# Optimization experiments

Measured on AMD Instinct MI355X. Metric: run time of the kernel, lower is better.

The kernel has to match this reference:

```python
import jax, jax.numpy as jnp
import numpy as np

B, L, H, NH = 8, 1024, 1024, 16
HD = H // NH  # head_dim = 64
SCALE = HD ** -0.5


def setup_inputs() -> dict:
    key = jax.random.key(0)
    kx, kqkv, kw, kb = jax.random.split(key, 4)
    x = jax.random.normal(kx, (B, L, H), dtype=jnp.float32)
    # nn.Linear(H, 3H, bias=False): weight [3H, H]
    w_qkv = jax.random.normal(kqkv, (3 * H, H), dtype=jnp.float32) * (H ** -0.5)
    # out_proj: nn.Linear(H, H) with bias
    w_out = jax.random.normal(kw, (H, H), dtype=jnp.float32) * (H ** -0.5)
    b_out = jax.random.normal(kb, (H,), dtype=jnp.float32) * 0.01
    return {"x": x, "w_qkv": w_qkv, "w_out": w_out, "b_out": b_out}


def reference(x, w_qkv, w_out, b_out):
    # qkv projection: [B, L, 3H]
    qkv = jnp.einsum('bld,ed->ble', x, w_qkv)
    # rearrange 'b l (qkv h d) -> qkv b h l d'
    qkv = qkv.reshape(B, L, 3, NH, HD)
    q = qkv[:, :, 0].transpose(0, 2, 1, 3)  # [B, NH, L, HD]
    k = qkv[:, :, 1].transpose(0, 2, 1, 3)
    v = qkv[:, :, 2].transpose(0, 2, 1, 3)
    att = jnp.einsum('bhxd,bhyd->bhxy', q, k) * SCALE
    att = jax.nn.softmax(att, axis=-1)
    o = jnp.einsum('bhxy,bhyd->bhxd', att, v)  # [B, NH, L, HD]
    o = o.transpose(0, 2, 1, 3).reshape(B, L, H)
    return jnp.einsum('bld,ed->ble', o, w_out) + b_out
```

## Files before the change

### kernel.cpp

```cpp
#include <hip/hip_runtime.h>


typedef short s16x8 __attribute__((ext_vector_type(8)));
typedef float f32x4 __attribute__((ext_vector_type(4)));
typedef unsigned int u32x2 __attribute__((ext_vector_type(2)));
typedef unsigned int u32x4 __attribute__((ext_vector_type(4)));

__device__ __forceinline__ unsigned short f2bf(float f) {
    union { float f; unsigned u; } c; c.f = f;
    return (unsigned short)((c.u + 0x7FFFu + ((c.u >> 16) & 1u)) >> 16);
}
__device__ __forceinline__ unsigned pack2bf(float a, float b) {
    union { float f; unsigned u; } ca, cb; ca.f = a; cb.f = b;
    return __builtin_amdgcn_perm(cb.u + 0x8000u, ca.u + 0x8000u, 0x07060302u);
}

#define GLOAD_LDS(g, l) __builtin_amdgcn_global_load_lds( \
    (const __attribute__((address_space(1))) void*)(g),   \
    (__attribute__((address_space(3))) void*)(l), 16, 0, 0)

__global__ __launch_bounds__(256) void cvt3(
    const float* __restrict__ s0, unsigned short* __restrict__ d0, int n0,
    const float* __restrict__ s1, unsigned short* __restrict__ d1, int n1,
    const float* __restrict__ s2, unsigned short* __restrict__ d2, int n2)
{
    long i = ((long)blockIdx.x * 256 + threadIdx.x) * 8;
    const float* s; unsigned short* d; long off;
    if (i < n0)                  { s = s0; d = d0; off = i; }
    else if (i < (long)n0 + n1)  { s = s1; d = d1; off = i - n0; }
    else                         { s = s2; d = d2; off = i - n0 - n1; }
    f32x4 a = *(const f32x4*)(s + off);
    f32x4 b = *(const f32x4*)(s + off + 4);
    u32x4 r;
    r[0] = pack2bf(a[0], a[1]); r[1] = pack2bf(a[2], a[3]);
    r[2] = pack2bf(b[0], b[1]); r[3] = pack2bf(b[2], b[3]);
    *(u32x4*)(d + off) = r;
}

template<int EPI>
__global__ __launch_bounds__(256) void gemm16(
    const unsigned short* __restrict__ A, const unsigned short* __restrict__ Bm,
    unsigned short* __restrict__ Cq, unsigned short* __restrict__ Cv,
    float* __restrict__ Cf, const float* __restrict__ bias,
    int N, int K)
{
    __shared__ unsigned short As[128 * 32];
    __shared__ unsigned short Bs[128 * 32];
    const int tid = threadIdx.x, lane = tid & 63, wave = tid >> 6;
    const int quad = lane >> 4, l16 = lane & 15;
    const int wm = (wave >> 1) * 64, wn = (wave & 1) * 64;
    const int m0 = blockIdx.y * 128, n0 = blockIdx.x * 128;

    const int lin0 = wave * 128 + lane, lin1 = lin0 + 64;
    const int r0 = lin0 >> 2, r1 = lin1 >> 2;
    const int q0c = (lin0 & 3) ^ ((r0 >> 1) & 3);
    const int q1c = (lin1 & 3) ^ ((r1 >> 1) & 3);
    const unsigned short* gA0 = A + (size_t)(m0 + r0) * K + q0c * 8;
    const unsigned short* gA1 = A + (size_t)(m0 + r1) * K + q1c * 8;
    const unsigned short* gB0 = Bm + (size_t)(n0 + r0) * K + q0c * 8;
    const unsigned short* gB1 = Bm + (size_t)(n0 + r1) * K + q1c * 8;

    const int pc = ((quad ^ ((l16 >> 1) & 3))) * 8;

    f32x4 acc[4][4] = {};
    for (int k0 = 0; k0 < K; k0 += 32) {
        __syncthreads();
        GLOAD_LDS(gA0, As + lin0 * 8);
        GLOAD_LDS(gA1, As + lin1 * 8);
        GLOAD_LDS(gB0, Bs + lin0 * 8);
        GLOAD_LDS(gB1, Bs + lin1 * 8);
        gA0 += 32; gA1 += 32; gB0 += 32; gB1 += 32;
        __syncthreads();
        s16x8 af[4], bf[4];
        #pragma unroll
        for (int i = 0; i < 4; ++i)
            af[i] = *(const s16x8*)(As + (wm + i * 16 + l16) * 32 + pc);
        #pragma unroll
        for (int j = 0; j < 4; ++j)
            bf[j] = *(const s16x8*)(Bs + (wn + j * 16 + l16) * 32 + pc);
        #pragma unroll
        for (int i = 0; i < 4; ++i)
            #pragma unroll
            for (int j = 0; j < 4; ++j)
                acc[i][j] = __builtin_amdgcn_mfma_f32_16x16x32_bf16(af[i], bf[j], acc[i][j], 0, 0, 0);
    }

    if (EPI == 1) {
        #pragma unroll
        for (int j = 0; j < 4; ++j) {
            int col = n0 + wn + j * 16 + l16;
            float bv = bias[col];
            #pragma unroll
            for (int i = 0; i < 4; ++i)
                #pragma unroll
                for (int r = 0; r < 4; ++r)
                    Cf[(size_t)(m0 + wm + i * 16 + quad * 4 + r) * N + col] = acc[i][j][r] + bv;
        }
    } else if (n0 < 2048) {
        #pragma unroll
        for (int j = 0; j < 4; ++j) {
            int col = n0 + wn + j * 16 + l16;
            #pragma unroll
            for (int i = 0; i < 4; ++i)
                #pragma unroll
                for (int r = 0; r < 4; ++r)
                    Cq[(size_t)(m0 + wm + i * 16 + quad * 4 + r) * 2048 + col] = f2bf(acc[i][j][r]);
        }
    } else {
        #pragma unroll
        for (int j = 0; j < 4; ++j) {
            int dcol = n0 + wn + j * 16 + l16 - 2048;
            int hh = dcol >> 6, dd = dcol & 63;
            #pragma unroll
            for (int i = 0; i < 4; ++i)
                #pragma unroll
                for (int r = 0; r < 4; ++r) {
                    int row = m0 + wm + i * 16 + quad * 4 + r;
                    int bb = row >> 10, l = row & 1023;
                    Cv[(size_t)((bb * 16 + hh) * 64 + dd) * 1024 + l] = f2bf(acc[i][j][r]);
                }
        }
    }
}

__global__ __launch_bounds__(256) void attn(
    const unsigned short* __restrict__ qk, const unsigned short* __restrict__ Vt,
    unsigned short* __restrict__ O)
{
    __shared__ unsigned short Ks[64 * 64];
    __shared__ unsigned short Vs[64 * 64];
    __shared__ unsigned short Ps[4][16 * 72];

    const int bh = blockIdx.y, b = bh >> 4, h = bh & 15;
    const int q0 = blockIdx.x * 64;
    const int tid = threadIdx.x, lane = tid & 63, wave = tid >> 6;
    const int quad = lane >> 4, l16 = lane & 15;

    const unsigned short* qrow = qk + (size_t)(b * 1024 + q0 + wave * 16 + l16) * 2048 + h * 64;
    s16x8 qf[2];
    qf[0] = *(const s16x8*)(qrow + quad * 8);
    qf[1] = *(const s16x8*)(qrow + 32 + quad * 8);

    const int rl = lane >> 3;
    const int qc = (lane & 7) ^ rl;
    const int g0 = wave * 2, g1 = g0 + 1;
    const unsigned short* srcK0 = qk + (size_t)(b * 1024 + g0 * 8 + rl) * 2048 + 1024 + h * 64 + qc * 8;
    const unsigned short* srcK1 = qk + (size_t)(b * 1024 + g1 * 8 + rl) * 2048 + 1024 + h * 64 + qc * 8;
    const unsigned short* srcV0 = Vt + (size_t)(bh * 64 + g0 * 8 + rl) * 1024 + qc * 8;
    const unsigned short* srcV1 = Vt + (size_t)(bh * 64 + g1 * 8 + rl) * 1024 + qc * 8;
    unsigned short* dK0 = Ks + g0 * 512 + lane * 8;
    unsigned short* dK1 = Ks + g1 * 512 + lane * 8;
    unsigned short* dV0 = Vs + g0 * 512 + lane * 8;
    unsigned short* dV1 = Vs + g1 * 512 + lane * 8;

    const int sw = l16 & 7;

    f32x4 Oacc[4] = {};
    float lsum = 0.0f;

    for (int kv = 0; kv < 1024; kv += 64) {
        __syncthreads();
        GLOAD_LDS(srcK0, dK0);
        GLOAD_LDS(srcK1, dK1);
        GLOAD_LDS(srcV0, dV0);
        GLOAD_LDS(srcV1, dV1);
        srcK0 += (size_t)64 * 2048; srcK1 += (size_t)64 * 2048;
        srcV0 += 64; srcV1 += 64;
        __syncthreads();

        f32x4 Sacc[4] = {};
        #pragma unroll
        for (int j = 0; j < 4; ++j) {
            #pragma unroll
            for (int s = 0; s < 2; ++s) {
                s16x8 kf = *(const s16x8*)(Ks + (j * 16 + l16) * 64 + (((s * 4 + quad) ^ sw)) * 8);
                Sacc[j] = __builtin_amdgcn_mfma_f32_16x16x32_bf16(kf, qf[s], Sacc[j], 0, 0, 0);
            }
        }

        #pragma unroll
        for (int j = 0; j < 4; ++j) {
            float p0 = __expf(Sacc[j][0] * 0.125f);
            float p1 = __expf(Sacc[j][1] * 0.125f);
            float p2 = __expf(Sacc[j][2] * 0.125f);
            float p3 = __expf(Sacc[j][3] * 0.125f);
            lsum += (p0 + p1) + (p2 + p3);
            u32x2 pw;
            pw[0] = pack2bf(p0, p1);
            pw[1] = pack2bf(p2, p3);
            *(u32x2*)(Ps[wave] + l16 * 72 + j * 16 + quad * 4) = pw;
        }
        asm volatile("s_waitcnt lgkmcnt(0)" ::: "memory");

        #pragma unroll
        for (int s = 0; s < 2; ++s) {
            s16x8 pf = *(const s16x8*)(Ps[wave] + l16 * 72 + s * 32 + quad * 8);
            #pragma unroll
            for (int j = 0; j < 4; ++j) {
                s16x8 vf = *(const s16x8*)(Vs + (j * 16 + l16) * 64 + (((s * 4 + quad) ^ sw)) * 8);
                Oacc[j] = __builtin_amdgcn_mfma_f32_16x16x32_bf16(pf, vf, Oacc[j], 0, 0, 0);
            }
        }
    }

    lsum += __shfl_xor(lsum, 16, 64);
    lsum += __shfl_xor(lsum, 32, 64);
    float rinv[4];
    #pragma unroll
    for (int r = 0; r < 4; ++r)
        rinv[r] = 1.0f / __shfl(lsum, quad * 4 + r, 64);

    #pragma unroll
    for (int j = 0; j < 4; ++j)
        #pragma unroll
        for (int r = 0; r < 4; ++r) {
            int row = q0 + wave * 16 + quad * 4 + r;
            int col = h * 64 + j * 16 + l16;
            O[(size_t)(b * 1024 + row) * 1024 + col] = f2bf(Oacc[j][r] * rinv[r]);
        }
}

extern "C" void kernel_launch(void* const* d_in, const int* in_sizes, int n_in,
                              void* d_out, int out_size, void* d_ws, size_t ws_size,
                              hipStream_t stream) {
    const float* x     = (const float*)d_in[0];
    const float* w_qkv = (const float*)d_in[1];
    const float* w_out = (const float*)d_in[2];
    const float* b_out = (const float*)d_in[3];
    float* out = (float*)d_out;

    const int nx = 8192 * 1024, nwq = 3072 * 1024, nwo = 1024 * 1024;
    unsigned short* xb  = (unsigned short*)d_ws;
    unsigned short* wqb = xb + nx;
    unsigned short* wob = wqb + nwq;
    unsigned short* qkb = wob + nwo;
    unsigned short* Vt  = qkb + (size_t)8192 * 2048;
    unsigned short* Ob  = xb;

    dim3 blk(256);
    cvt3<<<6144, blk, 0, stream>>>(x, xb, nx, w_qkv, wqb, nwq, w_out, wob, nwo);
    gemm16<0><<<dim3(24, 64), blk, 0, stream>>>(xb, wqb, qkb, Vt, nullptr, nullptr, 3072, 1024);
    attn<<<dim3(16, 128), blk, 0, stream>>>(qkb, Vt, Ob);
    gemm16<1><<<dim3(8, 64), blk, 0, stream>>>(Ob, wob, nullptr, nullptr, out, b_out, 1024, 1024);
}
```

Baseline: 256.2 us.

## Deepen GEMM K-tile, double attention query rows per block, vectorize V stores

The GEMM kernel now stages a K-slice of 64 instead of 32 per iteration, using an 8-way XOR swizzle. This halves the number of barrier pairs and gives more MFMA work per sync. The attention kernel processes 128 query rows per block, two 64-row halves per wave, so each K/V tile loaded into LDS is reused twice and the grid shrinks to half the blocks. The transposed V epilogue packs four bf16 values into one 8-byte store. In exchange, shared memory and register use go up, which may lower occupancy.

```diff
diff --git a/kernel.cpp b/kernel.cpp
--- a/kernel.cpp
+++ b/kernel.cpp
@@ -44,45 +44,50 @@
     float* __restrict__ Cf, const float* __restrict__ bias,
     int N, int K)
 {
-    __shared__ unsigned short As[128 * 32];
-    __shared__ unsigned short Bs[128 * 32];
+    __shared__ unsigned short As[128 * 64];
+    __shared__ unsigned short Bs[128 * 64];
     const int tid = threadIdx.x, lane = tid & 63, wave = tid >> 6;
     const int quad = lane >> 4, l16 = lane & 15;
     const int wm = (wave >> 1) * 64, wn = (wave & 1) * 64;
     const int m0 = blockIdx.y * 128, n0 = blockIdx.x * 128;
 
-    const int lin0 = wave * 128 + lane, lin1 = lin0 + 64;
-    const int r0 = lin0 >> 2, r1 = lin1 >> 2;
-    const int q0c = (lin0 & 3) ^ ((r0 >> 1) & 3);
-    const int q1c = (lin1 & 3) ^ ((r1 >> 1) & 3);
-    const unsigned short* gA0 = A + (size_t)(m0 + r0) * K + q0c * 8;
-    const unsigned short* gA1 = A + (size_t)(m0 + r1) * K + q1c * 8;
-    const unsigned short* gB0 = Bm + (size_t)(n0 + r0) * K + q0c * 8;
-    const unsigned short* gB1 = Bm + (size_t)(n0 + r1) * K + q1c * 8;
-
-    const int pc = ((quad ^ ((l16 >> 1) & 3))) * 8;
+    const int prow = tid >> 3;
+    const int qch  = (tid & 7) ^ (prow & 7);
+    const unsigned short* gA[4];
+    const unsigned short* gB[4];
+    #pragma unroll
+    for (int c = 0; c < 4; ++c) {
+        gA[c] = A + (size_t)(m0 + c * 32 + prow) * K + qch * 8;
+        gB[c] = Bm + (size_t)(n0 + c * 32 + prow) * K + qch * 8;
+    }
+    const int sw = l16 & 7;
 
     f32x4 acc[4][4] = {};
-    for (int k0 = 0; k0 < K; k0 += 32) {
-        __syncthreads();
-        GLOAD_LDS(gA0, As + lin0 * 8);
-        GLOAD_LDS(gA1, As + lin1 * 8);
-        GLOAD_LDS(gB0, Bs + lin0 * 8);
-        GLOAD_LDS(gB1, Bs + lin1 * 8);
-        gA0 += 32; gA1 += 32; gB0 += 32; gB1 += 32;
-        __syncthreads();
-        s16x8 af[4], bf[4];
-        #pragma unroll
-        for (int i = 0; i < 4; ++i)
-            af[i] = *(const s16x8*)(As + (wm + i * 16 + l16) * 32 + pc);
-        #pragma unroll
-        for (int j = 0; j < 4; ++j)
-            bf[j] = *(const s16x8*)(Bs + (wn + j * 16 + l16) * 32 + pc);
-        #pragma unroll
-        for (int i = 0; i < 4; ++i)
+    for (int k0 = 0; k0 < K; k0 += 64) {
+        __syncthreads();
+        #pragma unroll
+        for (int c = 0; c < 4; ++c) {
+            GLOAD_LDS(gA[c], As + (c * 256 + tid) * 8);
+            GLOAD_LDS(gB[c], Bs + (c * 256 + tid) * 8);
+            gA[c] += 64; gB[c] += 64;
+        }
+        __syncthreads();
+        #pragma unroll
+        for (int s = 0; s < 2; ++s) {
+            s16x8 af[4], bf[4];
+            const int pc = ((s * 4 + quad) ^ sw) * 8;
+            #pragma unroll
+            for (int i = 0; i < 4; ++i)
+                af[i] = *(const s16x8*)(As + (wm + i * 16 + l16) * 64 + pc);
             #pragma unroll
             for (int j = 0; j < 4; ++j)
-                acc[i][j] = __builtin_amdgcn_mfma_f32_16x16x32_bf16(af[i], bf[j], acc[i][j], 0, 0, 0);
+                bf[j] = *(const s16x8*)(Bs + (wn + j * 16 + l16) * 64 + pc);
+            #pragma unroll
+            for (int i = 0; i < 4; ++i)
+                #pragma unroll
+                for (int j = 0; j < 4; ++j)
+                    acc[i][j] = __builtin_amdgcn_mfma_f32_16x16x32_bf16(af[i], bf[j], acc[i][j], 0, 0, 0);
+        }
     }
 
     if (EPI == 1) {
@@ -112,13 +117,14 @@
             int dcol = n0 + wn + j * 16 + l16 - 2048;
             int hh = dcol >> 6, dd = dcol & 63;
             #pragma unroll
-            for (int i = 0; i < 4; ++i)
-                #pragma unroll
-                for (int r = 0; r < 4; ++r) {
-                    int row = m0 + wm + i * 16 + quad * 4 + r;
-                    int bb = row >> 10, l = row & 1023;
-                    Cv[(size_t)((bb * 16 + hh) * 64 + dd) * 1024 + l] = f2bf(acc[i][j][r]);
-                }
+            for (int i = 0; i < 4; ++i) {
+                int row = m0 + wm + i * 16 + quad * 4;
+                int bb = row >> 10, l = row & 1023;
+                u32x2 pw;
+                pw[0] = pack2bf(acc[i][j][0], acc[i][j][1]);
+                pw[1] = pack2bf(acc[i][j][2], acc[i][j][3]);
+                *(u32x2*)(Cv + (size_t)((bb * 16 + hh) * 64 + dd) * 1024 + l) = pw;
+            }
         }
     }
 }
@@ -129,23 +135,27 @@
 {
     __shared__ unsigned short Ks[64 * 64];
     __shared__ unsigned short Vs[64 * 64];
-    __shared__ unsigned short Ps[4][16 * 72];
-
-    const int bh = blockIdx.y, b = bh >> 4, h = bh & 15;
-    const int q0 = blockIdx.x * 64;
+    __shared__ unsigned short Ps[4][2][16 * 72];
+
+    const int bh = blockIdx.y, b = bh >> 4, hh = bh & 15;
+    const int q0 = blockIdx.x * 128;
     const int tid = threadIdx.x, lane = tid & 63, wave = tid >> 6;
     const int quad = lane >> 4, l16 = lane & 15;
 
-    const unsigned short* qrow = qk + (size_t)(b * 1024 + q0 + wave * 16 + l16) * 2048 + h * 64;
-    s16x8 qf[2];
-    qf[0] = *(const s16x8*)(qrow + quad * 8);
-    qf[1] = *(const s16x8*)(qrow + 32 + quad * 8);
+    s16x8 qf[2][2];
+    #pragma unroll
+    for (int h = 0; h < 2; ++h) {
+        const unsigned short* qrow =
+            qk + (size_t)(b * 1024 + q0 + h * 64 + wave * 16 + l16) * 2048 + hh * 64;
+        qf[h][0] = *(const s16x8*)(qrow + quad * 8);
+        qf[h][1] = *(const s16x8*)(qrow + 32 + quad * 8);
+    }
 
     const int rl = lane >> 3;
     const int qc = (lane & 7) ^ rl;
     const int g0 = wave * 2, g1 = g0 + 1;
-    const unsigned short* srcK0 = qk + (size_t)(b * 1024 + g0 * 8 + rl) * 2048 + 1024 + h * 64 + qc * 8;
-    const unsigned short* srcK1 = qk + (size_t)(b * 1024 + g1 * 8 + rl) * 2048 + 1024 + h * 64 + qc * 8;
+    const unsigned short* srcK0 = qk + (size_t)(b * 1024 + g0 * 8 + rl) * 2048 + 1024 + hh * 64 + qc * 8;
+    const unsigned short* srcK1 = qk + (size_t)(b * 1024 + g1 * 8 + rl) * 2048 + 1024 + hh * 64 + qc * 8;
     const unsigned short* srcV0 = Vt + (size_t)(bh * 64 + g0 * 8 + rl) * 1024 + qc * 8;
     const unsigned short* srcV1 = Vt + (size_t)(bh * 64 + g1 * 8 + rl) * 1024 + qc * 8;
     unsigned short* dK0 = Ks + g0 * 512 + lane * 8;
@@ -155,8 +165,8 @@
 
     const int sw = l16 & 7;
 
-    f32x4 Oacc[4] = {};
-    float lsum = 0.0f;
+    f32x4 Oacc[2][4] = {};
+    float lsum[2] = {0.0f, 0.0f};
 
     for (int kv = 0; kv < 1024; kv += 64) {
         __syncthreads();
@@ -168,56 +178,61 @@
         srcV0 += 64; srcV1 += 64;
         __syncthreads();
 
-        f32x4 Sacc[4] = {};
-        #pragma unroll
-        for (int j = 0; j < 4; ++j) {
+        #pragma unroll
+        for (int h = 0; h < 2; ++h) {
+            unsigned short* Pw = &Ps[wave][h][0];
+            f32x4 Sacc[4] = {};
+            #pragma unroll
+            for (int j = 0; j < 4; ++j) {
+                #pragma unroll
+                for (int s = 0; s < 2; ++s) {
+                    s16x8 kf = *(const s16x8*)(Ks + (j * 16 + l16) * 64 + ((s * 4 + quad) ^ sw) * 8);
+                    Sacc[j] = __builtin_amdgcn_mfma_f32_16x16x32_bf16(kf, qf[h][s], Sacc[j], 0, 0, 0);
+                }
+            }
+            #pragma unroll
+            for (int j = 0; j < 4; ++j) {
+                float p0 = __expf(Sacc[j][0] * 0.125f);
+                float p1 = __expf(Sacc[j][1] * 0.125f);
+                float p2 = __expf(Sacc[j][2] * 0.125f);
+                float p3 = __expf(Sacc[j][3] * 0.125f);
+                lsum[h] += (p0 + p1) + (p2 + p3);
+                u32x2 pw;
+                pw[0] = pack2bf(p0, p1);
+                pw[1] = pack2bf(p2, p3);
+                *(u32x2*)(Pw + l16 * 72 + j * 16 + quad * 4) = pw;
+            }
+            asm volatile("s_waitcnt lgkmcnt(0)" ::: "memory");
             #pragma unroll
             for (int s = 0; s < 2; ++s) {
-                s16x8 kf = *(const s16x8*)(Ks + (j * 16 + l16) * 64 + (((s * 4 + quad) ^ sw)) * 8);
-                Sacc[j] = __builtin_amdgcn_mfma_f32_16x16x32_bf16(kf, qf[s], Sacc[j], 0, 0, 0);
-            }
-        }
-
-        #pragma unroll
-        for (int j = 0; j < 4; ++j) {
-            float p0 = __expf(Sacc[j][0] * 0.125f);
-            float p1 = __expf(Sacc[j][1] * 0.125f);
-            float p2 = __expf(Sacc[j][2] * 0.125f);
-            float p3 = __expf(Sacc[j][3] * 0.125f);
-            lsum += (p0 + p1) + (p2 + p3);
-            u32x2 pw;
-            pw[0] = pack2bf(p0, p1);
-            pw[1] = pack2bf(p2, p3);
-            *(u32x2*)(Ps[wave] + l16 * 72 + j * 16 + quad * 4) = pw;
-        }
-        asm volatile("s_waitcnt lgkmcnt(0)" ::: "memory");
-
-        #pragma unroll
-        for (int s = 0; s < 2; ++s) {
-            s16x8 pf = *(const s16x8*)(Ps[wave] + l16 * 72 + s * 32 + quad * 8);
-            #pragma unroll
-            for (int j = 0; j < 4; ++j) {
-                s16x8 vf = *(const s16x8*)(Vs + (j * 16 + l16) * 64 + (((s * 4 + quad) ^ sw)) * 8);
-                Oacc[j] = __builtin_amdgcn_mfma_f32_16x16x32_bf16(pf, vf, Oacc[j], 0, 0, 0);
-            }
-        }
-    }
-
-    lsum += __shfl_xor(lsum, 16, 64);
-    lsum += __shfl_xor(lsum, 32, 64);
-    float rinv[4];
+                s16x8 pf = *(const s16x8*)(Pw + l16 * 72 + s * 32 + quad * 8);
+                #pragma unroll
+                for (int j = 0; j < 4; ++j) {
+                    s16x8 vf = *(const s16x8*)(Vs + (j * 16 + l16) * 64 + ((s * 4 + quad) ^ sw) * 8);
+                    Oacc[h][j] = __builtin_amdgcn_mfma_f32_16x16x32_bf16(pf, vf, Oacc[h][j], 0, 0, 0);
+                }
+            }
+        }
+    }
+
     #pragma unroll
-    for (int r = 0; r < 4; ++r)
-        rinv[r] = 1.0f / __shfl(lsum, quad * 4 + r, 64);
-
-    #pragma unroll
-    for (int j = 0; j < 4; ++j)
-        #pragma unroll
-        for (int r = 0; r < 4; ++r) {
-            int row = q0 + wave * 16 + quad * 4 + r;
-            int col = h * 64 + j * 16 + l16;
-            O[(size_t)(b * 1024 + row) * 1024 + col] = f2bf(Oacc[j][r] * rinv[r]);
-        }
+    for (int h = 0; h < 2; ++h) {
+        float ls = lsum[h];
+        ls += __shfl_xor(ls, 16, 64);
+        ls += __shfl_xor(ls, 32, 64);
+        float rinv[4];
+        #pragma unroll
+        for (int r = 0; r < 4; ++r)
+            rinv[r] = 1.0f / __shfl(ls, quad * 4 + r, 64);
+        #pragma unroll
+        for (int j = 0; j < 4; ++j)
+            #pragma unroll
+            for (int r = 0; r < 4; ++r) {
+                int row = q0 + h * 64 + wave * 16 + quad * 4 + r;
+                int col = hh * 64 + j * 16 + l16;
+                O[(size_t)(b * 1024 + row) * 1024 + col] = f2bf(Oacc[h][j][r] * rinv[r]);
+            }
+    }
 }
 
 extern "C" void kernel_launch(void* const* d_in, const int* in_sizes, int n_in,
@@ -240,6 +255,6 @@
     dim3 blk(256);
     cvt3<<<6144, blk, 0, stream>>>(x, xb, nx, w_qkv, wqb, nwq, w_out, wob, nwo);
     gemm16<0><<<dim3(24, 64), blk, 0, stream>>>(xb, wqb, qkb, Vt, nullptr, nullptr, 3072, 1024);
-    attn<<<dim3(16, 128), blk, 0, stream>>>(qkb, Vt, Ob);
+    attn<<<dim3(8, 128), blk, 0, stream>>>(qkb, Vt, Ob);
     gemm16<1><<<dim3(8, 64), blk, 0, stream>>>(Ob, wob, nullptr, nullptr, out, b_out, 1024, 1024);
 }
```

Measured after the change: 243.1 us. 5.1% less time.
